# Optimization experiments

Measured on AMD Instinct MI355X. Metric: run time of the kernel, lower is better.

The kernel has to match this reference:

```python
import jax, jax.numpy as jnp
import numpy as np

D = 32        # dmodel (forced by reshape(..., 32) in the original)
N = 2000      # n_nodes == liner_fourth
SLOPE = 0.2   # LeakyReLU negative slope
EPS = 1e-6    # SublayerConnection LayerNorm eps (annotated-transformer style)


def _layernorm(x, g, b):
    m = x.mean(-1, keepdims=True)
    v = x.var(-1, keepdims=True)
    return g * (x - m) / jnp.sqrt(v + EPS) + b


def setup_inputs() -> dict:
    key = jax.random.key(0)
    ks = jax.random.split(key, 18)
    F_, NL, NS = 16, 500, 1500
    s = 0.1
    return {
        "state": jax.random.normal(ks[0], (F_, NS, D), jnp.float32),
        "left": jax.random.normal(ks[1], (F_, NL, D), jnp.float32),
        "inputad": jax.random.bernoulli(ks[2], 0.02, (F_, N, N)).astype(jnp.float32),
        "w3": s * jax.random.normal(ks[3], (D, D), jnp.float32),       # linearThird
        "b3": jnp.zeros((D,), jnp.float32),
        "attn_w": s * jax.random.normal(ks[4], (1, 2 * D), jnp.float32),  # attn (no bias)
        "w4": s * jax.random.normal(ks[5], (D, N), jnp.float32),       # linearFourth: 2000->32
        "b4": jnp.zeros((D,), jnp.float32),
        "w1": s * jax.random.normal(ks[6], (D, D), jnp.float32),       # linear
        "b1": jnp.zeros((D,), jnp.float32),
        "w_ih": s * jax.random.normal(ks[7], (4 * D, D), jnp.float32),  # LSTMCell (gate order i,f,g,o)
        "w_hh": s * jax.random.normal(ks[8], (4 * D, D), jnp.float32),
        "b_ih": jnp.zeros((4 * D,), jnp.float32),
        "b_hh": jnp.zeros((4 * D,), jnp.float32),
        "ln_g": jnp.ones((D,), jnp.float32),                            # SublayerConnection norm
        "ln_b": jnp.zeros((D,), jnp.float32),
        "w2": s * jax.random.normal(ks[9], (D, D), jnp.float32),        # linearSecond
        "b2": jnp.zeros((D,), jnp.float32),
    }


def reference(state, left, inputad, w3, b3, attn_w, w4, b4, w1, b1,
              w_ih, w_hh, b_ih, b_hh, ln_g, ln_b, w2, b2):
    # eval mode: all dropouts are identity
    x = jnp.concatenate([left, state], axis=1)          # [F, N, D]
    F_, n = x.shape[0], x.shape[1]
    g = x @ w3.T + b3                                   # [F, N, D]

    # torch: e = leaky(attn(cat([g.repeat_interleave(n,0), g.repeat(n,1,1)], -1)))
    # Decompose the linear over the concat: attn_w = [a_l | a_r].
    # g_repeat_interleave row m -> g[m // n]; g_repeat row m -> g[m % F_];
    # e.view(F_, n, n)[b, i, j] = e_flat[b*n + i, j].
    a_l, a_r = attn_w[0, :D], attn_w[0, D:]
    s_l = g @ a_l                                        # [F, N]
    s_r = g @ a_r                                        # [F, N]
    idx = (jnp.arange(F_)[:, None] * n + jnp.arange(n)[None, :]) % F_  # [F, N]
    e_mat = jax.nn.leaky_relu(s_l[:, None, :] + s_r[idx], SLOPE)       # [F, N, N]

    e_masked = jnp.where(inputad == 0, 0.0, e_mat)       # masked_fill(adj==0, 0)
    h = jax.nn.leaky_relu(jnp.einsum('bij,oj->bio', e_masked, w4) + b4, SLOPE)  # [F, N, 32]

    # first softmax(e)/dropout pair is dead code (overwritten); a = softmax(h, dim=1)
    a = jax.nn.softmax(h, axis=1)
    st = (a * g) @ w1.T + b1                             # elementwise branch (a.shape == g.shape)

    agg = jnp.matmul(inputad, st)                        # bmm(degree2, state): [F, N, D]

    # SublayerConnection: st + dropout(sublayer(norm(st))); sublayer = LSTMCell cell-state
    nx = _layernorm(st, ln_g, ln_b)
    c0 = nx.reshape(-1, D)                               # initial cell state = norm(st)
    # h0 = zeros, so the w_hh @ h0 contribution vanishes (b_hh still applies)
    gates = agg.reshape(-1, D) @ w_ih.T + b_ih + b_hh    # [F*N, 4D]
    i_g = jax.nn.sigmoid(gates[:, :D])
    f_g = jax.nn.sigmoid(gates[:, D:2 * D])
    g_g = jnp.tanh(gates[:, 2 * D:3 * D])
    c1 = f_g * c0 + i_g * g_g                            # LSTMCell returns (h', c'); [1] -> c'

    out = st + c1.reshape(F_, n, D)
    return out @ w2.T + b2
```

## Files before the change

### kernel.cpp

```cpp
#include <hip/hip_runtime.h>
#include <math.h>

#define F_    16
#define NROW  2000
#define NL    500
#define D     32
#define ROWS  (F_*NROW)
#define SLOPE 0.2f
#define CAP   128
#define LCAP  256

__global__ __launch_bounds__(256) void k1_g(
    const float* __restrict__ state, const float* __restrict__ left,
    const float* __restrict__ w3, const float* __restrict__ b3,
    const float* __restrict__ attn_w,
    float* __restrict__ g, float* __restrict__ s_l, float* __restrict__ s_r)
{
    __shared__ float sw3[D*D];
    __shared__ float sb3[D], sal[D], sar[D];
    int t = threadIdx.x;
    for (int k = t; k < D*D; k += 256) sw3[k] = w3[k];
    if (t < D) { sb3[t] = b3[t]; sal[t] = attn_w[t]; sar[t] = attn_w[D + t]; }
    __syncthreads();
    int row = blockIdx.x * 256 + t;
    if (row >= ROWS) return;
    int b = row / NROW, i = row - b * NROW;
    const float* xrow = (i < NL) ? (left  + ((size_t)b * NL + i) * D)
                                 : (state + ((size_t)b * (NROW - NL) + (i - NL)) * D);
    float x[D];
#pragma unroll
    for (int k = 0; k < D/4; ++k) {
        float4 v = reinterpret_cast<const float4*>(xrow)[k];
        x[4*k] = v.x; x[4*k+1] = v.y; x[4*k+2] = v.z; x[4*k+3] = v.w;
    }
    float sl = 0.f, sr = 0.f;
    float ob[4];
    float* grow = g + (size_t)row * D;
#pragma unroll
    for (int d = 0; d < D; ++d) {
        float acc = sb3[d];
#pragma unroll
        for (int k = 0; k < D; ++k) acc += x[k] * sw3[d*D + k];
        sl += acc * sal[d]; sr += acc * sar[d];
        ob[d & 3] = acc;
        if ((d & 3) == 3)
            reinterpret_cast<float4*>(grow)[d >> 2] = make_float4(ob[0], ob[1], ob[2], ob[3]);
    }
    s_l[row] = sl; s_r[row] = sr;
}

__global__ __launch_bounds__(256) void k1b_w4t(const float* __restrict__ w4,
                                               float* __restrict__ w4t)
{
    int t = blockIdx.x * 256 + threadIdx.x;
    if (t < D * NROW) {
        int o = t / NROW, j = t - o * NROW;
        w4t[j * D + o] = w4[t];
    }
}

__global__ __launch_bounds__(256) void k2_scan(
    const float* __restrict__ adj,
    const float* __restrict__ s_l, const float* __restrict__ s_r,
    const float* __restrict__ w4t, const float* __restrict__ b4,
    float* __restrict__ h, int* __restrict__ nzc, unsigned short* __restrict__ nzi)
{
    __shared__ int   sh_j[4][LCAP];
    __shared__ float sh_e[4][LCAP];
    int t = threadIdx.x;
    int w = t >> 6, lane = t & 63;
    int row = blockIdx.x * 4 + w;
    int b = row / NROW, i = row - b * NROW;
    int r = i & 15;
    const float4* mrow = reinterpret_cast<const float4*>(adj + (size_t)row * NROW);
    unsigned long long lmask = (1ull << lane) - 1ull;
    int cnt = 0;
#pragma unroll
    for (int it = 0; it < 8; ++it) {
        int idx4 = it * 64 + lane;
        float4 v = make_float4(0.f, 0.f, 0.f, 0.f);
        if (idx4 < NROW/4) v = mrow[idx4];
#pragma unroll
        for (int c = 0; c < 4; ++c) {
            float val = (c == 0) ? v.x : (c == 1) ? v.y : (c == 2) ? v.z : v.w;
            bool p = (val != 0.0f);
            unsigned long long m = __ballot(p);
            if (p) {
                int pos = cnt + __popcll(m & lmask);
                if (pos < LCAP) sh_j[w][pos] = idx4 * 4 + c;
            }
            cnt += __popcll(m);
        }
    }
    if (cnt > LCAP) cnt = LCAP;
    __syncthreads();
    const float* slb = s_l + (size_t)b * NROW;
    const float* srr = s_r + (size_t)r * NROW;
    for (int k = lane; k < cnt; k += 64) {
        int j = sh_j[w][k];
        float e = slb[j] + srr[j];
        sh_e[w][k] = (e > 0.f) ? e : SLOPE * e;
    }
    __syncthreads();
    int o = lane & 31, half = lane >> 5;
    float acc = 0.f;
    for (int k = half; k < cnt; k += 2)
        acc += sh_e[w][k] * w4t[sh_j[w][k] * D + o];
    acc += __shfl_xor(acc, 32, 64);
    if (lane < 32) {
        float hv = acc + b4[o];
        h[(size_t)row * D + o] = (hv > 0.f) ? hv : SLOPE * hv;
    }
    int cc = (cnt < CAP) ? cnt : CAP;
    for (int k = lane; k < cc; k += 64)
        nzi[(size_t)row * CAP + k] = (unsigned short)sh_j[w][k];
    if (lane == 0) nzc[row] = cc;
}

__global__ __launch_bounds__(256) void k3a_psum(const float* __restrict__ h,
                                                float* __restrict__ psum)
{
    int b = blockIdx.x, slice = blockIdx.y;
    int t = threadIdx.x;
    int o = t & 31, ti = t >> 5;
    int base = slice * 250;
    float s = 0.f;
    for (int i = base + ti; i < base + 250; i += 8)
        s += expf(h[((size_t)b * NROW + i) * D + o]);
    __shared__ float red[8][D];
    red[ti][o] = s;
    __syncthreads();
    if (t < D) {
        float tot = 0.f;
#pragma unroll
        for (int k = 0; k < 8; ++k) tot += red[k][t];
        psum[((size_t)b * 8 + slice) * D + t] = tot;
    }
}

__global__ __launch_bounds__(256) void k3b_st(
    const float* __restrict__ h, const float* __restrict__ g,
    const float* __restrict__ psum,
    const float* __restrict__ w1, const float* __restrict__ b1,
    float* __restrict__ st)
{
    __shared__ float sw1[D*D], sb1[D], ssum[D];
    int t = threadIdx.x;
    int b = blockIdx.y, chunk = blockIdx.x;
    for (int k = t; k < D*D; k += 256) sw1[k] = w1[k];
    if (t < D) {
        sb1[t] = b1[t];
        float tot = 0.f;
#pragma unroll
        for (int s = 0; s < 8; ++s) tot += psum[((size_t)b * 8 + s) * D + t];
        ssum[t] = tot;
    }
    __syncthreads();
    if (t >= 250) return;
    size_t row = (size_t)b * NROW + chunk * 250 + t;
    const float* hrow = h + row * D;
    const float* grow = g + row * D;
    float p[D];
#pragma unroll
    for (int k = 0; k < D; ++k)
        p[k] = (expf(hrow[k]) / ssum[k]) * grow[k];
    float* strow = st + row * D;
    float ob[4];
#pragma unroll
    for (int d = 0; d < D; ++d) {
        float acc = sb1[d];
#pragma unroll
        for (int k = 0; k < D; ++k) acc += p[k] * sw1[d*D + k];
        ob[d & 3] = acc;
        if ((d & 3) == 3)
            reinterpret_cast<float4*>(strow)[d >> 2] = make_float4(ob[0], ob[1], ob[2], ob[3]);
    }
}

__global__ __launch_bounds__(256) void k4_final(
    const float* __restrict__ st,
    const int* __restrict__ nzc, const unsigned short* __restrict__ nzi,
    const float* __restrict__ w_ih, const float* __restrict__ b_ih,
    const float* __restrict__ b_hh,
    const float* __restrict__ ln_g, const float* __restrict__ ln_b,
    const float* __restrict__ w2, const float* __restrict__ b2,
    float* __restrict__ out)
{
    __shared__ float swih[96*33];
    __shared__ float sw2[D*33];
    __shared__ float sbg[96];
    __shared__ float sb2[D], slg[D], slb[D];
    __shared__ unsigned short jl[8][CAP];
    __shared__ float aggsh[8][D];
    __shared__ float s2sh[8][D];

    int t = threadIdx.x;
    for (int k = t; k < 96*D; k += 256) swih[(k/D)*33 + (k%D)] = w_ih[k];
    for (int k = t; k < D*D;  k += 256) sw2 [(k/D)*33 + (k%D)] = w2[k];
    if (t < 96) sbg[t] = b_ih[t] + b_hh[t];
    if (t < D) { sb2[t] = b2[t]; slg[t] = ln_g[t]; slb[t] = ln_b[t]; }

    int grp = t >> 5, lane = t & 31;
    int row = blockIdx.x * 8 + grp;
    int b = row / NROW;
    int cnt = nzc[row];
    const unsigned short* lst = nzi + (size_t)row * CAP;
    for (int k = lane; k < cnt; k += 32) jl[grp][k] = lst[k];
    __syncthreads();

    const float* stb = st + (size_t)b * NROW * D;
    float agg = 0.f;
    int k = 0;
    for (; k + 4 <= cnt; k += 4) {
        int j0 = jl[grp][k], j1 = jl[grp][k+1], j2 = jl[grp][k+2], j3 = jl[grp][k+3];
        float a0 = stb[j0*D + lane], a1 = stb[j1*D + lane];
        float a2 = stb[j2*D + lane], a3 = stb[j3*D + lane];
        agg += (a0 + a1) + (a2 + a3);
    }
    for (; k < cnt; ++k) agg += stb[jl[grp][k]*D + lane];

    float sv = st[(size_t)row * D + lane];

    float sum = sv;
#pragma unroll
    for (int m = 16; m >= 1; m >>= 1) sum += __shfl_xor(sum, m, 32);
    float mean = sum * (1.f / D);
    float dd = sv - mean;
    float vs = dd * dd;
#pragma unroll
    for (int m = 16; m >= 1; m >>= 1) vs += __shfl_xor(vs, m, 32);
    float inv = 1.f / sqrtf(vs * (1.f / D) + 1e-6f);
    float nx = slg[lane] * dd * inv + slb[lane];

    aggsh[grp][lane] = agg;
    __syncthreads();

    float gi = sbg[lane], gf = sbg[lane + 32], gg = sbg[lane + 64];
#pragma unroll
    for (int d = 0; d < D; ++d) {
        float a = aggsh[grp][d];
        gi += swih[lane*33 + d]      * a;
        gf += swih[(lane+32)*33 + d] * a;
        gg += swih[(lane+64)*33 + d] * a;
    }
    float ig  = 1.f / (1.f + expf(-gi));
    float fg  = 1.f / (1.f + expf(-gf));
    float g_g = tanhf(gg);
    float s2  = sv + fg * nx + ig * g_g;

    s2sh[grp][lane] = s2;
    __syncthreads();

    float acc = sb2[lane];
#pragma unroll
    for (int q = 0; q < D; ++q) acc += sw2[lane*33 + q] * s2sh[grp][q];
    out[(size_t)row * D + lane] = acc;
}

extern "C" void kernel_launch(void* const* d_in, const int* in_sizes, int n_in,
                              void* d_out, int out_size, void* d_ws, size_t ws_size,
                              hipStream_t stream)
{
    const float* state  = (const float*)d_in[0];
    const float* left   = (const float*)d_in[1];
    const float* adj    = (const float*)d_in[2];
    const float* w3     = (const float*)d_in[3];
    const float* b3     = (const float*)d_in[4];
    const float* attn_w = (const float*)d_in[5];
    const float* w4     = (const float*)d_in[6];
    const float* b4     = (const float*)d_in[7];
    const float* w1     = (const float*)d_in[8];
    const float* b1     = (const float*)d_in[9];
    const float* w_ih   = (const float*)d_in[10];
    const float* b_ih   = (const float*)d_in[12];
    const float* b_hh   = (const float*)d_in[13];
    const float* ln_g   = (const float*)d_in[14];
    const float* ln_b   = (const float*)d_in[15];
    const float* w2     = (const float*)d_in[16];
    const float* b2     = (const float*)d_in[17];
    float* out = (float*)d_out;

    float* g    = (float*)d_ws;
    float* h    = g  + (size_t)ROWS * D;
    float* st   = h  + (size_t)ROWS * D;
    float* s_l  = st + (size_t)ROWS * D;
    float* s_r  = s_l + ROWS;
    float* w4t  = s_r + ROWS;
    float* psum = w4t + (size_t)NROW * D;
    int*   nzc  = (int*)(psum + F_ * 8 * D);
    unsigned short* nzi = (unsigned short*)(nzc + ROWS);

    k1_g   <<<dim3(ROWS/256),           dim3(256), 0, stream>>>(state, left, w3, b3, attn_w, g, s_l, s_r);
    k1b_w4t<<<dim3((D*NROW+255)/256),   dim3(256), 0, stream>>>(w4, w4t);
    k2_scan<<<dim3(ROWS/4),             dim3(256), 0, stream>>>(adj, s_l, s_r, w4t, b4, h, nzc, nzi);
    k3a_psum<<<dim3(F_, 8),             dim3(256), 0, stream>>>(h, psum);
    k3b_st <<<dim3(8, F_),              dim3(256), 0, stream>>>(h, g, psum, w1, b1, st);
    k4_final<<<dim3(ROWS/8),            dim3(256), 0, stream>>>(st, nzc, nzi, w_ih, b_ih, b_hh,
                                                                ln_g, ln_b, w2, b2, out);
}
```

Measured before the change: 153.0 us.

## Use warp-per-row shuffle matvecs, fuse w4 transpose into k1, drop intra-wave syncs

Rewrites the g and st projection kernels to assign one 32-lane group per row, broadcasting inputs with shuffles against a padded shared weight matrix, which spreads more work across the GPU. The w4 transpose is folded into the first kernel as extra blocks to save a launch. The psum reduction doubles its slice count, and block barriers are removed where data is only shared within one wavefront. This relies on wavefront lockstep for correctness of the shared-memory exchanges.

```diff
diff --git a/kernel.cpp b/kernel.cpp
--- a/kernel.cpp
+++ b/kernel.cpp
@@ -13,50 +13,43 @@
 __global__ __launch_bounds__(256) void k1_g(
     const float* __restrict__ state, const float* __restrict__ left,
     const float* __restrict__ w3, const float* __restrict__ b3,
-    const float* __restrict__ attn_w,
-    float* __restrict__ g, float* __restrict__ s_l, float* __restrict__ s_r)
-{
-    __shared__ float sw3[D*D];
+    const float* __restrict__ attn_w, const float* __restrict__ w4,
+    float* __restrict__ g, float* __restrict__ s_l, float* __restrict__ s_r,
+    float* __restrict__ w4t)
+{
+    int bid = blockIdx.x;
+    int t = threadIdx.x;
+    if (bid >= ROWS/8) {
+        int k = (bid - ROWS/8) * 256 + t;
+        if (k < D * NROW) {
+            int o = k / NROW, j = k - o * NROW;
+            w4t[j * D + o] = w4[k];
+        }
+        return;
+    }
+    __shared__ float sw3[D*33];
     __shared__ float sb3[D], sal[D], sar[D];
-    int t = threadIdx.x;
-    for (int k = t; k < D*D; k += 256) sw3[k] = w3[k];
+    for (int k = t; k < D*D; k += 256) sw3[(k>>5)*33 + (k&31)] = w3[k];
     if (t < D) { sb3[t] = b3[t]; sal[t] = attn_w[t]; sar[t] = attn_w[D + t]; }
     __syncthreads();
-    int row = blockIdx.x * 256 + t;
-    if (row >= ROWS) return;
+    int grp = t >> 5, lane = t & 31;
+    int row = bid * 8 + grp;
     int b = row / NROW, i = row - b * NROW;
     const float* xrow = (i < NL) ? (left  + ((size_t)b * NL + i) * D)
                                  : (state + ((size_t)b * (NROW - NL) + (i - NL)) * D);
-    float x[D];
-#pragma unroll
-    for (int k = 0; k < D/4; ++k) {
-        float4 v = reinterpret_cast<const float4*>(xrow)[k];
-        x[4*k] = v.x; x[4*k+1] = v.y; x[4*k+2] = v.z; x[4*k+3] = v.w;
-    }
-    float sl = 0.f, sr = 0.f;
-    float ob[4];
-    float* grow = g + (size_t)row * D;
-#pragma unroll
-    for (int d = 0; d < D; ++d) {
-        float acc = sb3[d];
-#pragma unroll
-        for (int k = 0; k < D; ++k) acc += x[k] * sw3[d*D + k];
-        sl += acc * sal[d]; sr += acc * sar[d];
-        ob[d & 3] = acc;
-        if ((d & 3) == 3)
-            reinterpret_cast<float4*>(grow)[d >> 2] = make_float4(ob[0], ob[1], ob[2], ob[3]);
-    }
-    s_l[row] = sl; s_r[row] = sr;
-}
-
-__global__ __launch_bounds__(256) void k1b_w4t(const float* __restrict__ w4,
-                                               float* __restrict__ w4t)
-{
-    int t = blockIdx.x * 256 + threadIdx.x;
-    if (t < D * NROW) {
-        int o = t / NROW, j = t - o * NROW;
-        w4t[j * D + o] = w4[t];
-    }
+    float x = xrow[lane];
+    float acc = sb3[lane];
+#pragma unroll
+    for (int k = 0; k < D; ++k)
+        acc += __shfl(x, k, 32) * sw3[lane*33 + k];
+    g[(size_t)row * D + lane] = acc;
+    float pl = acc * sal[lane], pr = acc * sar[lane];
+#pragma unroll
+    for (int m = 16; m >= 1; m >>= 1) {
+        pl += __shfl_xor(pl, m, 32);
+        pr += __shfl_xor(pr, m, 32);
+    }
+    if (lane == 0) { s_l[row] = pl; s_r[row] = pr; }
 }
 
 __global__ __launch_bounds__(256) void k2_scan(
@@ -93,7 +86,6 @@
         }
     }
     if (cnt > LCAP) cnt = LCAP;
-    __syncthreads();
     const float* slb = s_l + (size_t)b * NROW;
     const float* srr = s_r + (size_t)r * NROW;
     for (int k = lane; k < cnt; k += 64) {
@@ -101,7 +93,6 @@
         float e = slb[j] + srr[j];
         sh_e[w][k] = (e > 0.f) ? e : SLOPE * e;
     }
-    __syncthreads();
     int o = lane & 31, half = lane >> 5;
     float acc = 0.f;
     for (int k = half; k < cnt; k += 2)
@@ -123,9 +114,9 @@
     int b = blockIdx.x, slice = blockIdx.y;
     int t = threadIdx.x;
     int o = t & 31, ti = t >> 5;
-    int base = slice * 250;
+    int base = slice * 125;
     float s = 0.f;
-    for (int i = base + ti; i < base + 250; i += 8)
+    for (int i = base + ti; i < base + 125; i += 8)
         s += expf(h[((size_t)b * NROW + i) * D + o]);
     __shared__ float red[8][D];
     red[ti][o] = s;
@@ -134,7 +125,7 @@
         float tot = 0.f;
 #pragma unroll
         for (int k = 0; k < 8; ++k) tot += red[k][t];
-        psum[((size_t)b * 8 + slice) * D + t] = tot;
+        psum[((size_t)b * 16 + slice) * D + t] = tot;
     }
 }
 
@@ -144,37 +135,27 @@
     const float* __restrict__ w1, const float* __restrict__ b1,
     float* __restrict__ st)
 {
-    __shared__ float sw1[D*D], sb1[D], ssum[D];
-    int t = threadIdx.x;
-    int b = blockIdx.y, chunk = blockIdx.x;
-    for (int k = t; k < D*D; k += 256) sw1[k] = w1[k];
+    __shared__ float sw1[D*33], sb1[D], ssum[D];
+    int t = threadIdx.x;
+    int bid = blockIdx.x;
+    int b = bid / 250;
+    for (int k = t; k < D*D; k += 256) sw1[(k>>5)*33 + (k&31)] = w1[k];
     if (t < D) {
         sb1[t] = b1[t];
         float tot = 0.f;
 #pragma unroll
-        for (int s = 0; s < 8; ++s) tot += psum[((size_t)b * 8 + s) * D + t];
+        for (int s = 0; s < 16; ++s) tot += psum[((size_t)b * 16 + s) * D + t];
         ssum[t] = tot;
     }
     __syncthreads();
-    if (t >= 250) return;
-    size_t row = (size_t)b * NROW + chunk * 250 + t;
-    const float* hrow = h + row * D;
-    const float* grow = g + row * D;
-    float p[D];
+    int grp = t >> 5, lane = t & 31;
+    size_t row = (size_t)bid * 8 + grp;
+    float p = (expf(h[row * D + lane]) / ssum[lane]) * g[row * D + lane];
+    float acc = sb1[lane];
 #pragma unroll
     for (int k = 0; k < D; ++k)
-        p[k] = (expf(hrow[k]) / ssum[k]) * grow[k];
-    float* strow = st + row * D;
-    float ob[4];
-#pragma unroll
-    for (int d = 0; d < D; ++d) {
-        float acc = sb1[d];
-#pragma unroll
-        for (int k = 0; k < D; ++k) acc += p[k] * sw1[d*D + k];
-        ob[d & 3] = acc;
-        if ((d & 3) == 3)
-            reinterpret_cast<float4*>(strow)[d >> 2] = make_float4(ob[0], ob[1], ob[2], ob[3]);
-    }
+        acc += __shfl(p, k, 32) * sw1[lane*33 + k];
+    st[row * D + lane] = acc;
 }
 
 __global__ __launch_bounds__(256) void k4_final(
@@ -233,7 +214,6 @@
     float nx = slg[lane] * dd * inv + slb[lane];
 
     aggsh[grp][lane] = agg;
-    __syncthreads();
 
     float gi = sbg[lane], gf = sbg[lane + 32], gg = sbg[lane + 64];
 #pragma unroll
@@ -249,7 +229,6 @@
     float s2  = sv + fg * nx + ig * g_g;
 
     s2sh[grp][lane] = s2;
-    __syncthreads();
 
     float acc = sb2[lane];
 #pragma unroll
@@ -287,14 +266,14 @@
     float* s_r  = s_l + ROWS;
     float* w4t  = s_r + ROWS;
     float* psum = w4t + (size_t)NROW * D;
-    int*   nzc  = (int*)(psum + F_ * 8 * D);
+    int*   nzc  = (int*)(psum + F_ * 16 * D);
     unsigned short* nzi = (unsigned short*)(nzc + ROWS);
 
-    k1_g   <<<dim3(ROWS/256),           dim3(256), 0, stream>>>(state, left, w3, b3, attn_w, g, s_l, s_r);
-    k1b_w4t<<<dim3((D*NROW+255)/256),   dim3(256), 0, stream>>>(w4, w4t);
-    k2_scan<<<dim3(ROWS/4),             dim3(256), 0, stream>>>(adj, s_l, s_r, w4t, b4, h, nzc, nzi);
-    k3a_psum<<<dim3(F_, 8),             dim3(256), 0, stream>>>(h, psum);
-    k3b_st <<<dim3(8, F_),              dim3(256), 0, stream>>>(h, g, psum, w1, b1, st);
-    k4_final<<<dim3(ROWS/8),            dim3(256), 0, stream>>>(st, nzc, nzi, w_ih, b_ih, b_hh,
-                                                                ln_g, ln_b, w2, b2, out);
-}
+    k1_g    <<<dim3(ROWS/8 + (D*NROW+255)/256), dim3(256), 0, stream>>>(
+                state, left, w3, b3, attn_w, w4, g, s_l, s_r, w4t);
+    k2_scan <<<dim3(ROWS/4),  dim3(256), 0, stream>>>(adj, s_l, s_r, w4t, b4, h, nzc, nzi);
+    k3a_psum<<<dim3(F_, 16),  dim3(256), 0, stream>>>(h, psum);
+    k3b_st  <<<dim3(ROWS/8),  dim3(256), 0, stream>>>(h, g, psum, w1, b1, st);
+    k4_final<<<dim3(ROWS/8),  dim3(256), 0, stream>>>(st, nzc, nzi, w_ih, b_ih, b_hh,
+                                                      ln_g, ln_b, w2, b2, out);
+}
```

Result: faster. 141.8 us (-7.4%).
